# Kernel tuning notes

Measured on AMD Instinct MI355X. Metric: run time of the kernel, lower is better.

## Reference

```python
import jax, jax.numpy as jnp
import numpy as np

B, T, C = 2, 2048, 1024
NH = 16
HS = C // NH            # 64
BD = max(HS // 4, 16)   # 16
HORIZON = 32


def _windows(t, delta):
    # t: [B, nh, T, d] -> [B, nh, T, delta, d]; window w at pos i maps to original index i-delta+1+w
    padded = jnp.pad(t, ((0, 0), (0, 0), (delta - 1, 0), (0, 0)))
    idx = jnp.arange(t.shape[2])[:, None] + jnp.arange(delta)[None, :]
    return padded[:, :, idx]


def setup_inputs() -> dict:
    key = jax.random.key(0)
    ks = jax.random.split(key, 16)
    s = 0.02
    inp = {
        "x": jax.random.normal(ks[0], (B, T, C), dtype=jnp.float32),
        # weights stored [in, out] (transposed vs torch Linear)
        "w_disp": jax.random.normal(ks[1], (C, NH * BD), dtype=jnp.float32) * s,
        "b_disp": jnp.zeros((NH * BD,), dtype=jnp.float32),
        "w_val": jax.random.normal(ks[2], (C, C), dtype=jnp.float32) * s,
        "b_val": jnp.zeros((C,), dtype=jnp.float32),
        "rel_pos_emb": jax.random.normal(ks[3], (HORIZON, BD), dtype=jnp.float32) * s,
        "w_state": jax.random.normal(ks[4], (BD, BD), dtype=jnp.float32) * s,
        "b_state": jnp.zeros((BD,), dtype=jnp.float32),
        "w_strain": jax.random.normal(ks[5], (BD, BD), dtype=jnp.float32) * s,
        "b_strain": jnp.zeros((BD,), dtype=jnp.float32),
        "w_state_i": jax.random.normal(ks[6], (BD, BD), dtype=jnp.float32) * s,
        "w_state_j": jax.random.normal(ks[7], (BD, BD), dtype=jnp.float32) * s,
        "w_pos": jax.random.normal(ks[8], (BD, BD), dtype=jnp.float32) * s,
        "w_bond_out": jax.random.normal(ks[9], (BD, 1), dtype=jnp.float32) * s,
        "b_bond_out": jnp.zeros((1,), dtype=jnp.float32),
        "w_damage": jax.random.normal(ks[10], (BD, BD), dtype=jnp.float32) * s,
        "b_damage": jnp.zeros((BD,), dtype=jnp.float32),
        "w_damage_out": jax.random.normal(ks[11], (BD, 1), dtype=jnp.float32) * s,
        "b_damage_out": jnp.full((1,), -3.0, dtype=jnp.float32),
        "w_cproj": jax.random.normal(ks[12], (C, C), dtype=jnp.float32) * s,
        "b_cproj": jnp.zeros((C,), dtype=jnp.float32),
    }
    return inp


def reference(x, w_disp, b_disp, w_val, b_val, rel_pos_emb, w_state, b_state,
              w_strain, b_strain, w_state_i, w_state_j, w_pos,
              w_bond_out, b_bond_out, w_damage, b_damage,
              w_damage_out, b_damage_out, w_cproj, b_cproj):
    Bx, Tx, Cx = x.shape
    delta = min(HORIZON, Tx)
    gelu = lambda v: jax.nn.gelu(v, approximate=False)

    disp = (x @ w_disp + b_disp).reshape(Bx, Tx, NH, BD).transpose(0, 2, 1, 3)   # [B,nh,T,bd]
    val = (x @ w_val + b_val).reshape(Bx, Tx, NH, HS).transpose(0, 2, 1, 3)      # [B,nh,T,hs]

    disp_win = _windows(disp, delta)    # [B,nh,T,delta,bd]
    val_win = _windows(val, delta)      # [B,nh,T,delta,hs]

    cmask = (jnp.arange(Tx)[:, None] - delta + 1 + jnp.arange(delta)[None, :]) >= 0  # [T,delta]
    cmask_f = cmask.astype(x.dtype)

    strain = disp_win - disp[:, :, :, None, :]                                   # [B,nh,T,delta,bd]
    strain_for_state = strain @ w_state + b_state
    valid_counts = jnp.clip(cmask_f.sum(axis=-1), 1.0)                           # [T]
    state = (strain_for_state * cmask_f[None, None, :, :, None]).sum(axis=3) \
            / valid_counts[None, None, :, None]                                  # [B,nh,T,bd]
    state_win = _windows(state, delta)                                           # [B,nh,T,delta,bd]

    rel_emb = rel_pos_emb[:delta]                                                # [delta,bd]
    bond_act = gelu(strain @ w_strain + b_strain
                    + state[:, :, :, None, :] @ w_state_i
                    + state_win @ w_state_j
                    + rel_emb @ w_pos)                                           # [B,nh,T,delta,bd]
    bond_logits = (bond_act @ w_bond_out)[..., 0] + b_bond_out[0]                # [B,nh,T,delta]

    damage_act = gelu(strain @ w_damage + b_damage)
    damage = jax.nn.sigmoid((damage_act @ w_damage_out)[..., 0] + b_damage_out[0])

    logits = bond_logits - damage * 10.0
    logits = jnp.where(cmask[None, None], logits, -jnp.inf)
    weights = jax.nn.softmax(logits, axis=-1)                                    # [B,nh,T,delta]

    out = jnp.einsum('bntd,bntde->bnte', weights, val_win)                       # [B,nh,T,hs]
    out = out.transpose(0, 2, 1, 3).reshape(Bx, Tx, Cx)
    return out @ w_cproj + b_cproj
```

## Files before the change

### kernel.cpp

```cpp
#include <hip/hip_runtime.h>
#include <hip/hip_bf16.h>
#include <math.h>

constexpr int B_ = 2, T_ = 2048, C_ = 1024, NH_ = 16, HS_ = 64, BD_ = 16, DELTA_ = 32;
constexpr int M_ = B_ * T_;

typedef __bf16 bf16_t;
typedef __bf16 bf16x8 __attribute__((ext_vector_type(8)));
typedef float  f32x4  __attribute__((ext_vector_type(4)));

__device__ __forceinline__ float gelu_f(float x) {
    const float u = 0.7978845608028654f * (x + 0.044715f * x * x * x);
    const float e = __expf(2.0f * u);
    const float th = 1.0f - 2.0f / (e + 1.0f);
    return 0.5f * x * (1.0f + th);
}

__global__ __launch_bounds__(256) void convert_bf16_kernel(
    const float* __restrict__ in, bf16_t* __restrict__ out, int n)
{
    const int i = (blockIdx.x * 256 + threadIdx.x) * 8;
    if (i >= n) return;
    const float4 v0 = *(const float4*)(in + i);
    const float4 v1 = *(const float4*)(in + i + 4);
    bf16x8 o;
    o[0] = (bf16_t)v0.x; o[1] = (bf16_t)v0.y; o[2] = (bf16_t)v0.z; o[3] = (bf16_t)v0.w;
    o[4] = (bf16_t)v1.x; o[5] = (bf16_t)v1.y; o[6] = (bf16_t)v1.z; o[7] = (bf16_t)v1.w;
    *(bf16x8*)(out + i) = o;
}

__global__ __launch_bounds__(256) void transpose_w_kernel(
    const float* __restrict__ in, bf16_t* __restrict__ out, int K, int N)
{
    __shared__ float tile[32][33];
    const int n0 = blockIdx.x * 32, k0 = blockIdx.y * 32;
    const int tx = threadIdx.x & 31, ty = threadIdx.x >> 5;
    #pragma unroll
    for (int i = 0; i < 4; ++i)
        tile[ty + 8 * i][tx] = in[(size_t)(k0 + ty + 8 * i) * N + n0 + tx];
    __syncthreads();
    #pragma unroll
    for (int i = 0; i < 4; ++i)
        out[(size_t)(n0 + ty + 8 * i) * K + k0 + tx] = (bf16_t)tile[tx][ty + 8 * i];
}

__device__ __forceinline__ void gload16(const void* g, void* l) {
    __builtin_amdgcn_global_load_lds(
        (__attribute__((address_space(1))) void*)(g),
        (__attribute__((address_space(3))) void*)(l), 16, 0, 0);
}

#define GBM 128
#define GBN 64
#define GBK 32
__global__ __launch_bounds__(256) void gemm_bf16_async(
    const bf16_t* __restrict__ A, const bf16_t* __restrict__ Bt,
    const float* __restrict__ bias, float* __restrict__ C,
    int M, int N, int K)
{
    __shared__ __align__(16) bf16_t Al[GBM][GBK];
    __shared__ __align__(16) bf16_t Bl[GBN][GBK];
    const int tid  = threadIdx.x;
    const int lane = tid & 63;
    const int w    = tid >> 6;
    const int wr   = w >> 1, wc = w & 1;
    const int bm   = blockIdx.y * GBM, bn = blockIdx.x * GBN;

    const int lrow = lane >> 2;
    const int lcol = (lane & 3) * 8;
    const bf16_t* Ag0 = A  + (size_t)(bm + w * 32 + lrow) * K + lcol;
    const bf16_t* Ag1 = Ag0 + (size_t)16 * K;
    const bf16_t* Bg  = Bt + (size_t)(bn + w * 16 + lrow) * K + lcol;

    f32x4 acc[4][2] = {};

    for (int k0 = 0; k0 < K; k0 += GBK) {
        gload16(Ag0 + k0, &Al[w * 32][0]);
        gload16(Ag1 + k0, &Al[w * 32 + 16][0]);
        gload16(Bg  + k0, &Bl[w * 16][0]);
        __syncthreads();
        bf16x8 af[4], bf2[2];
        #pragma unroll
        for (int i = 0; i < 4; ++i)
            af[i] = *(const bf16x8*)&Al[wr * 64 + i * 16 + (lane & 15)][(lane >> 4) * 8];
        #pragma unroll
        for (int j = 0; j < 2; ++j)
            bf2[j] = *(const bf16x8*)&Bl[wc * 32 + j * 16 + (lane & 15)][(lane >> 4) * 8];
        #pragma unroll
        for (int i = 0; i < 4; ++i)
            #pragma unroll
            for (int j = 0; j < 2; ++j)
                acc[i][j] = __builtin_amdgcn_mfma_f32_16x16x32_bf16(af[i], bf2[j], acc[i][j], 0, 0, 0);
        __syncthreads();
    }

    #pragma unroll
    for (int i = 0; i < 4; ++i) {
        const int r0 = bm + wr * 64 + i * 16 + (lane >> 4) * 4;
        #pragma unroll
        for (int j = 0; j < 2; ++j) {
            const int c = bn + wc * 32 + j * 16 + (lane & 15);
            const float bv = bias[c];
            float* cp = C + (size_t)r0 * N + c;
            #pragma unroll
            for (int q = 0; q < 4; ++q)
                cp[(size_t)q * N] = acc[i][j][q] + bv;
        }
    }
}

#define PCT 128
__global__ __launch_bounds__(256) void precomp_kernel(
    const float* __restrict__ disp,
    const float* __restrict__ w_state, const float* __restrict__ b_state,
    const float* __restrict__ w_strain, const float* __restrict__ b_strain,
    const float* __restrict__ w_state_i, const float* __restrict__ w_state_j,
    const float* __restrict__ w_damage,
    float* __restrict__ P1, float* __restrict__ Q1, float* __restrict__ P2)
{
    __shared__ float s_d[PCT + 31][20];
    __shared__ float s_mv[PCT][20];
    __shared__ float s_st[PCT][20];
    __shared__ float s_wst[16][16], s_wstr[16][16], s_wsi[16][16], s_wsj[16][16], s_wdmg[16][16];
    __shared__ float s_bst[16], s_bstr[16];

    const int bid = blockIdx.x;
    const int tile = bid & (T_ / PCT - 1);
    const int h    = (bid >> 4) & 15;
    const int b    = bid >> 8;
    const int t0   = tile * PCT;
    const int tid  = threadIdx.x;

    s_wst[tid >> 4][tid & 15]  = w_state[tid];
    s_wstr[tid >> 4][tid & 15] = w_strain[tid];
    s_wsi[tid >> 4][tid & 15]  = w_state_i[tid];
    s_wsj[tid >> 4][tid & 15]  = w_state_j[tid];
    s_wdmg[tid >> 4][tid & 15] = w_damage[tid];
    if (tid < 16) { s_bst[tid] = b_state[tid]; s_bstr[tid] = b_strain[tid]; }

    for (int it = tid; it < (PCT + 31) * 4; it += 256) {
        const int row = it >> 2, q = it & 3;
        int rg = t0 - 31 + row; if (rg < 0) rg = 0;
        *(float4*)&s_d[row][q * 4] =
            *(const float4*)(disp + (size_t)(b * T_ + rg) * 256 + h * 16 + q * 4);
    }
    __syncthreads();

    #pragma unroll
    for (int p = 0; p < 8; ++p) {
        const int it = p * 256 + tid;
        const int tl = it >> 4, e = it & 15;
        const int t = t0 + tl;
        const int dlo = max(0, 31 - t);
        float s = 0.0f;
        for (int d = dlo; d < 32; ++d) s += s_d[tl + d][e];
        s_mv[tl][e] = s / (float)(32 - dlo) - s_d[tl + 31][e];
    }
    __syncthreads();

    #pragma unroll
    for (int p = 0; p < 8; ++p) {
        const int it = p * 256 + tid;
        const int tl = it >> 4, e = it & 15;
        float a = s_bst[e];
        #pragma unroll
        for (int k = 0; k < 16; ++k) a += s_mv[tl][k] * s_wst[k][e];
        s_st[tl][e] = a;
    }
    __syncthreads();

    #pragma unroll
    for (int p = 0; p < 8; ++p) {
        const int it = p * 256 + tid;
        const int tl = it >> 4, e = it & 15;
        float d1 = 0.0f, p2 = 0.0f, sj = 0.0f, si = 0.0f;
        #pragma unroll
        for (int k = 0; k < 16; ++k) {
            const float dv = s_d[tl + 31][k];
            const float sv = s_st[tl][k];
            d1 += dv * s_wstr[k][e];
            p2 += dv * s_wdmg[k][e];
            sj += sv * s_wsj[k][e];
            si += sv * s_wsi[k][e];
        }
        const size_t o = (size_t)(b * T_ + t0 + tl) * 256 + h * 16 + e;
        P1[o] = d1 + sj;
        Q1[o] = s_bstr[e] + si - d1;
        P2[o] = p2;
    }
}

__global__ __launch_bounds__(256) void attn_kernel(
    const float* __restrict__ P1, const float* __restrict__ Q1,
    const float* __restrict__ P2, const float* __restrict__ val,
    const float* __restrict__ rel_pos_emb, const float* __restrict__ w_pos,
    const float* __restrict__ w_bond_out, const float* __restrict__ b_bond_out,
    const float* __restrict__ b_damage,
    const float* __restrict__ w_damage_out, const float* __restrict__ b_damage_out,
    bf16_t* __restrict__ att)
{
    __shared__ float sP1[95][20], sP2[95][20], sQ1[64][20];
    __shared__ float sVal[95][68];
    __shared__ float sWv[64][33];
    __shared__ float s_relw[32][20];
    __shared__ float s_wb[16], s_wd[16], s_bd[16];

    const int tid  = threadIdx.x;
    const int bid  = blockIdx.x;
    const int tile = bid & 31;
    const int h    = (bid >> 5) & 15;
    const int b    = bid >> 9;
    const int t0   = tile * 64;

    for (int it = tid; it < 95 * 4; it += 256) {
        const int row = it >> 2, q = it & 3;
        int rg = t0 - 31 + row; if (rg < 0) rg = 0;
        const size_t o = (size_t)(b * T_ + rg) * 256 + h * 16 + q * 4;
        *(float4*)&sP1[row][q * 4] = *(const float4*)(P1 + o);
        *(float4*)&sP2[row][q * 4] = *(const float4*)(P2 + o);
    }
    {
        const int row = tid >> 2, q = tid & 3;
        *(float4*)&sQ1[row][q * 4] =
            *(const float4*)(Q1 + (size_t)(b * T_ + t0 + row) * 256 + h * 16 + q * 4);
    }
    for (int it = tid; it < 95 * 16; it += 256) {
        const int row = it >> 4, q = it & 15;
        int rg = t0 - 31 + row; if (rg < 0) rg = 0;
        *(float4*)&sVal[row][q * 4] =
            *(const float4*)(val + (size_t)(b * T_ + rg) * 1024 + h * 64 + q * 4);
    }
    {
        for (int it = tid; it < 512; it += 256) {
            const int dd = it >> 4, ee = it & 15;
            float a = 0.0f;
            #pragma unroll
            for (int k = 0; k < 16; ++k) a += rel_pos_emb[dd * 16 + k] * w_pos[k * 16 + ee];
            s_relw[dd][ee] = a;
        }
        if (tid < 16) {
            s_wb[tid] = w_bond_out[tid];
            s_wd[tid] = w_damage_out[tid];
            s_bd[tid] = b_damage[tid];
        }
    }
    __syncthreads();

    const int lane = tid & 63;
    const int w    = tid >> 6;
    const int half = lane >> 5;
    const int d    = lane & 31;
    const float bb  = b_bond_out[0];
    const float bdo = b_damage_out[0];

    #pragma unroll
    for (int pp = 0; pp < 8; ++pp) {
        const int p  = (w << 3) + pp;
        const int tl = (p << 1) + half;
        const int i  = tl + d;
        const bool valid = (t0 - 31 + i) >= 0;

        float bacc = 0.0f, dacc = 0.0f;
        #pragma unroll
        for (int q = 0; q < 4; ++q) {
            const float4 q1  = *(const float4*)&sQ1[tl][q * 4];
            const float4 p2t = *(const float4*)&sP2[tl + 31][q * 4];
            const float4 p1r = *(const float4*)&sP1[i][q * 4];
            const float4 p2r = *(const float4*)&sP2[i][q * 4];
            const float4 rw  = *(const float4*)&s_relw[d][q * 4];
            bacc += gelu_f(p1r.x + q1.x + rw.x) * s_wb[4 * q + 0];
            bacc += gelu_f(p1r.y + q1.y + rw.y) * s_wb[4 * q + 1];
            bacc += gelu_f(p1r.z + q1.z + rw.z) * s_wb[4 * q + 2];
            bacc += gelu_f(p1r.w + q1.w + rw.w) * s_wb[4 * q + 3];
            dacc += gelu_f(p2r.x - p2t.x + s_bd[4 * q + 0]) * s_wd[4 * q + 0];
            dacc += gelu_f(p2r.y - p2t.y + s_bd[4 * q + 1]) * s_wd[4 * q + 1];
            dacc += gelu_f(p2r.z - p2t.z + s_bd[4 * q + 2]) * s_wd[4 * q + 2];
            dacc += gelu_f(p2r.w - p2t.w + s_bd[4 * q + 3]) * s_wd[4 * q + 3];
        }

        float logit = -INFINITY;
        if (valid) {
            const float damage = 1.0f / (1.0f + __expf(-(dacc + bdo)));
            logit = bacc + bb - 10.0f * damage;
        }
        float m = logit;
        #pragma unroll
        for (int off = 16; off; off >>= 1) m = fmaxf(m, __shfl_xor(m, off, 32));
        const float pe = valid ? __expf(logit - m) : 0.0f;
        float ss = pe;
        #pragma unroll
        for (int off = 16; off; off >>= 1) ss += __shfl_xor(ss, off, 32);
        sWv[tl][d] = pe / ss;
    }

    #pragma unroll
    for (int pp = 0; pp < 8; ++pp) {
        const int tl0 = (w << 4) + (pp << 1);
        float acc0 = 0.0f, acc1 = 0.0f;
        #pragma unroll
        for (int j = 0; j < 33; ++j) {
            const float v = sVal[tl0 + j][lane];
            if (j < 32) acc0 += sWv[tl0][j] * v;
            if (j >= 1) acc1 += sWv[tl0 + 1][j - 1] * v;
        }
        const size_t o = (size_t)(b * T_ + t0 + tl0) * 1024 + h * 64 + lane;
        att[o]        = (bf16_t)acc0;
        att[o + 1024] = (bf16_t)acc1;
    }
}

extern "C" void kernel_launch(void* const* d_in, const int* in_sizes, int n_in,
                              void* d_out, int out_size, void* d_ws, size_t ws_size,
                              hipStream_t stream)
{
    const float* x        = (const float*)d_in[0];
    const float* w_disp   = (const float*)d_in[1];
    const float* b_disp   = (const float*)d_in[2];
    const float* w_val    = (const float*)d_in[3];
    const float* b_val    = (const float*)d_in[4];
    const float* rel      = (const float*)d_in[5];
    const float* w_state  = (const float*)d_in[6];
    const float* b_state  = (const float*)d_in[7];
    const float* w_strain = (const float*)d_in[8];
    const float* b_strain = (const float*)d_in[9];
    const float* w_si     = (const float*)d_in[10];
    const float* w_sj     = (const float*)d_in[11];
    const float* w_pos    = (const float*)d_in[12];
    const float* w_bond   = (const float*)d_in[13];
    const float* b_bond   = (const float*)d_in[14];
    const float* w_dmg    = (const float*)d_in[15];
    const float* b_dmg    = (const float*)d_in[16];
    const float* w_dout   = (const float*)d_in[17];
    const float* b_dout   = (const float*)d_in[18];
    const float* w_cproj  = (const float*)d_in[19];
    const float* b_cproj  = (const float*)d_in[20];

    float* out = (float*)d_out;
    float* ws  = (float*)d_ws;

    const size_t R = (size_t)M_ * 256;
    float* disp = ws;
    float* P1   = ws + R;
    float* Q1   = ws + 2 * R;
    float* P2   = ws + 3 * R;
    float* val  = ws + 4 * R;
    bf16_t* xb   = (bf16_t*)(ws + 8 * R);
    bf16_t* attb = xb;
    bf16_t* wdT  = (bf16_t*)(ws + 10 * R);
    bf16_t* wvT  = wdT + (size_t)256 * 1024;
    bf16_t* wcT  = wvT + (size_t)1024 * 1024;

    convert_bf16_kernel<<<(M_ * C_) / (256 * 8), 256, 0, stream>>>(x, xb, M_ * C_);
    transpose_w_kernel<<<dim3(256 / 32, C_ / 32), 256, 0, stream>>>(w_disp, wdT, C_, 256);
    transpose_w_kernel<<<dim3(C_ / 32, C_ / 32), 256, 0, stream>>>(w_val, wvT, C_, C_);
    transpose_w_kernel<<<dim3(C_ / 32, C_ / 32), 256, 0, stream>>>(w_cproj, wcT, C_, C_);

    gemm_bf16_async<<<dim3(256 / GBN, M_ / GBM), 256, 0, stream>>>(xb, wdT, b_disp, disp, M_, 256, C_);
    gemm_bf16_async<<<dim3(C_ / GBN, M_ / GBM), 256, 0, stream>>>(xb, wvT, b_val, val, M_, C_, C_);

    precomp_kernel<<<B_ * NH_ * (T_ / PCT), 256, 0, stream>>>(
        disp, w_state, b_state, w_strain, b_strain, w_si, w_sj, w_dmg, P1, Q1, P2);

    attn_kernel<<<B_ * NH_ * (T_ / 64), 256, 0, stream>>>(
        P1, Q1, P2, val, rel, w_pos, w_bond, b_bond, b_dmg, w_dout, b_dout, attb);

    gemm_bf16_async<<<dim3(C_ / GBN, M_ / GBM), 256, 0, stream>>>(attb, wcT, b_cproj, out, M_, C_, C_);
}
```

Measured before the change: 265.7 us.

## Double-buffer GEMMs, fuse disp/val GEMMs and transposes, use fast exp/rcp intrinsics

The GEMM now uses 128x128 tiles, double-buffered LDS with async prefetch of the next K tile, and an XCD-aware block remap. The disp and val projections become one launch, and the three weight transposes become one launch. GELU, sigmoid, softmax and the divisions switch to hardware exp2 and rcp intrinsics, with GELU rewritten in the form x*sigmoid. This cuts launch overhead, global-memory stalls and transcendental cost, at the price of doubling LDS use and slightly lower numerical precision.

```diff
diff --git a/kernel.cpp b/kernel.cpp
--- a/kernel.cpp
+++ b/kernel.cpp
@@ -9,12 +9,17 @@
 typedef __bf16 bf16x8 __attribute__((ext_vector_type(8)));
 typedef float  f32x4  __attribute__((ext_vector_type(4)));
 
+__device__ __forceinline__ float frcp(float x)  { return __builtin_amdgcn_rcpf(x); }
+__device__ __forceinline__ float fexp2(float x) { return __builtin_amdgcn_exp2f(x); }
+
 __device__ __forceinline__ float gelu_f(float x) {
-    const float u = 0.7978845608028654f * (x + 0.044715f * x * x * x);
-    const float e = __expf(2.0f * u);
-    const float th = 1.0f - 2.0f / (e + 1.0f);
-    return 0.5f * x * (1.0f + th);
-}
+    const float x2  = x * x;
+    const float arg = x * fmaf(0.10294321f, x2, 2.3022074f);
+    const float e   = fexp2(arg);
+    const float r   = frcp(e + 1.0f);
+    return x - x * r;
+}
+constexpr float LOG2E = 1.4426950409f;
 
 __global__ __launch_bounds__(256) void convert_bf16_kernel(
     const float* __restrict__ in, bf16_t* __restrict__ out, int n)
@@ -29,9 +34,17 @@
     *(bf16x8*)(out + i) = o;
 }
 
-__global__ __launch_bounds__(256) void transpose_w_kernel(
-    const float* __restrict__ in, bf16_t* __restrict__ out, int K, int N)
-{
+__global__ __launch_bounds__(256) void transpose3_kernel(
+    const float* __restrict__ w_val, const float* __restrict__ w_cproj,
+    const float* __restrict__ w_disp,
+    bf16_t* __restrict__ wvT, bf16_t* __restrict__ wcT, bf16_t* __restrict__ wdT)
+{
+    const int z = blockIdx.z;
+    const float* in; bf16_t* out; int K = 1024, N = 1024;
+    if (z == 0)      { in = w_val;   out = wvT; }
+    else if (z == 1) { in = w_cproj; out = wcT; }
+    else             { in = w_disp;  out = wdT; N = 256; if (blockIdx.x >= 8) return; }
+
     __shared__ float tile[32][33];
     const int n0 = blockIdx.x * 32, k0 = blockIdx.y * 32;
     const int tx = threadIdx.x & 31, ty = threadIdx.x >> 5;
@@ -51,55 +64,67 @@
 }
 
 #define GBM 128
-#define GBN 64
+#define GBN 128
 #define GBK 32
-__global__ __launch_bounds__(256) void gemm_bf16_async(
+
+__device__ __forceinline__ void gemm_core(
+    bf16_t (*Al)[GBM][GBK], bf16_t (*Bl)[GBN][GBK],
     const bf16_t* __restrict__ A, const bf16_t* __restrict__ Bt,
     const float* __restrict__ bias, float* __restrict__ C,
-    int M, int N, int K)
-{
-    __shared__ __align__(16) bf16_t Al[GBM][GBK];
-    __shared__ __align__(16) bf16_t Bl[GBN][GBK];
+    int N, int K, int bm, int bn)
+{
     const int tid  = threadIdx.x;
     const int lane = tid & 63;
     const int w    = tid >> 6;
     const int wr   = w >> 1, wc = w & 1;
-    const int bm   = blockIdx.y * GBM, bn = blockIdx.x * GBN;
 
     const int lrow = lane >> 2;
     const int lcol = (lane & 3) * 8;
     const bf16_t* Ag0 = A  + (size_t)(bm + w * 32 + lrow) * K + lcol;
     const bf16_t* Ag1 = Ag0 + (size_t)16 * K;
-    const bf16_t* Bg  = Bt + (size_t)(bn + w * 16 + lrow) * K + lcol;
-
-    f32x4 acc[4][2] = {};
-
-    for (int k0 = 0; k0 < K; k0 += GBK) {
-        gload16(Ag0 + k0, &Al[w * 32][0]);
-        gload16(Ag1 + k0, &Al[w * 32 + 16][0]);
-        gload16(Bg  + k0, &Bl[w * 16][0]);
-        __syncthreads();
-        bf16x8 af[4], bf2[2];
+    const bf16_t* Bg0 = Bt + (size_t)(bn + w * 32 + lrow) * K + lcol;
+    const bf16_t* Bg1 = Bg0 + (size_t)16 * K;
+
+    f32x4 acc[4][4] = {};
+    const int nt = K / GBK;
+    int cur = 0;
+
+    gload16(Ag0, &Al[0][w * 32][0]);
+    gload16(Ag1, &Al[0][w * 32 + 16][0]);
+    gload16(Bg0, &Bl[0][w * 32][0]);
+    gload16(Bg1, &Bl[0][w * 32 + 16][0]);
+    __syncthreads();
+
+    for (int t = 0; t < nt; ++t) {
+        if (t + 1 < nt) {
+            const int k1 = (t + 1) * GBK;
+            gload16(Ag0 + k1, &Al[cur ^ 1][w * 32][0]);
+            gload16(Ag1 + k1, &Al[cur ^ 1][w * 32 + 16][0]);
+            gload16(Bg0 + k1, &Bl[cur ^ 1][w * 32][0]);
+            gload16(Bg1 + k1, &Bl[cur ^ 1][w * 32 + 16][0]);
+        }
+        bf16x8 af[4], bfr[4];
         #pragma unroll
         for (int i = 0; i < 4; ++i)
-            af[i] = *(const bf16x8*)&Al[wr * 64 + i * 16 + (lane & 15)][(lane >> 4) * 8];
-        #pragma unroll
-        for (int j = 0; j < 2; ++j)
-            bf2[j] = *(const bf16x8*)&Bl[wc * 32 + j * 16 + (lane & 15)][(lane >> 4) * 8];
+            af[i] = *(const bf16x8*)&Al[cur][wr * 64 + i * 16 + (lane & 15)][(lane >> 4) * 8];
+        #pragma unroll
+        for (int j = 0; j < 4; ++j)
+            bfr[j] = *(const bf16x8*)&Bl[cur][wc * 64 + j * 16 + (lane & 15)][(lane >> 4) * 8];
         #pragma unroll
         for (int i = 0; i < 4; ++i)
             #pragma unroll
-            for (int j = 0; j < 2; ++j)
-                acc[i][j] = __builtin_amdgcn_mfma_f32_16x16x32_bf16(af[i], bf2[j], acc[i][j], 0, 0, 0);
+            for (int j = 0; j < 4; ++j)
+                acc[i][j] = __builtin_amdgcn_mfma_f32_16x16x32_bf16(af[i], bfr[j], acc[i][j], 0, 0, 0);
         __syncthreads();
+        cur ^= 1;
     }
 
     #pragma unroll
     for (int i = 0; i < 4; ++i) {
         const int r0 = bm + wr * 64 + i * 16 + (lane >> 4) * 4;
         #pragma unroll
-        for (int j = 0; j < 2; ++j) {
-            const int c = bn + wc * 32 + j * 16 + (lane & 15);
+        for (int j = 0; j < 4; ++j) {
+            const int c = bn + wc * 64 + j * 16 + (lane & 15);
             const float bv = bias[c];
             float* cp = C + (size_t)r0 * N + c;
             #pragma unroll
@@ -107,6 +132,40 @@
                 cp[(size_t)q * N] = acc[i][j][q] + bv;
         }
     }
+}
+
+__global__ __launch_bounds__(256) void gemm_bf16_db(
+    const bf16_t* __restrict__ A, const bf16_t* __restrict__ Bt,
+    const float* __restrict__ bias, float* __restrict__ C,
+    int M, int N, int K)
+{
+    __shared__ __align__(16) bf16_t Al[2][GBM][GBK];
+    __shared__ __align__(16) bf16_t Bl[2][GBN][GBK];
+    const int gx  = gridDim.x;
+    const int nwg = gx * gridDim.y;
+    const int bid = blockIdx.y * gx + blockIdx.x;
+    const int wid = (bid & 7) * (nwg >> 3) + (bid >> 3);
+    const int bx  = wid % gx, by = wid / gx;
+    gemm_core(Al, Bl, A, Bt, bias, C, N, K, by * GBM, bx * GBN);
+}
+
+__global__ __launch_bounds__(256) void gemm_dv_fused(
+    const bf16_t* __restrict__ A,
+    const bf16_t* __restrict__ wvT, const bf16_t* __restrict__ wdT,
+    const float* __restrict__ b_val, const float* __restrict__ b_disp,
+    float* __restrict__ val, float* __restrict__ disp)
+{
+    __shared__ __align__(16) bf16_t Al[2][GBM][GBK];
+    __shared__ __align__(16) bf16_t Bl[2][GBN][GBK];
+    const int gx  = 10;
+    const int nwg = 320;
+    const int bid = blockIdx.y * gx + blockIdx.x;
+    const int wid = (bid & 7) * (nwg >> 3) + (bid >> 3);
+    const int bx  = wid % gx, by = wid / gx;
+    if (bx < 8)
+        gemm_core(Al, Bl, A, wvT, b_val, val, 1024, 1024, by * GBM, bx * GBN);
+    else
+        gemm_core(Al, Bl, A, wdT, b_disp, disp, 256, 1024, by * GBM, (bx - 8) * GBN);
 }
 
 #define PCT 128
@@ -154,7 +213,7 @@
         const int dlo = max(0, 31 - t);
         float s = 0.0f;
         for (int d = dlo; d < 32; ++d) s += s_d[tl + d][e];
-        s_mv[tl][e] = s / (float)(32 - dlo) - s_d[tl + 31][e];
+        s_mv[tl][e] = s * frcp((float)(32 - dlo)) - s_d[tl + 31][e];
     }
     __syncthreads();
 
@@ -280,17 +339,17 @@
 
         float logit = -INFINITY;
         if (valid) {
-            const float damage = 1.0f / (1.0f + __expf(-(dacc + bdo)));
+            const float damage = frcp(1.0f + fexp2(-LOG2E * (dacc + bdo)));
             logit = bacc + bb - 10.0f * damage;
         }
         float m = logit;
         #pragma unroll
         for (int off = 16; off; off >>= 1) m = fmaxf(m, __shfl_xor(m, off, 32));
-        const float pe = valid ? __expf(logit - m) : 0.0f;
+        const float pe = valid ? fexp2(LOG2E * (logit - m)) : 0.0f;
         float ss = pe;
         #pragma unroll
         for (int off = 16; off; off >>= 1) ss += __shfl_xor(ss, off, 32);
-        sWv[tl][d] = pe / ss;
+        sWv[tl][d] = pe * frcp(ss);
     }
 
     #pragma unroll
@@ -351,12 +410,9 @@
     bf16_t* wcT  = wvT + (size_t)1024 * 1024;
 
     convert_bf16_kernel<<<(M_ * C_) / (256 * 8), 256, 0, stream>>>(x, xb, M_ * C_);
-    transpose_w_kernel<<<dim3(256 / 32, C_ / 32), 256, 0, stream>>>(w_disp, wdT, C_, 256);
-    transpose_w_kernel<<<dim3(C_ / 32, C_ / 32), 256, 0, stream>>>(w_val, wvT, C_, C_);
-    transpose_w_kernel<<<dim3(C_ / 32, C_ / 32), 256, 0, stream>>>(w_cproj, wcT, C_, C_);
-
-    gemm_bf16_async<<<dim3(256 / GBN, M_ / GBM), 256, 0, stream>>>(xb, wdT, b_disp, disp, M_, 256, C_);
-    gemm_bf16_async<<<dim3(C_ / GBN, M_ / GBM), 256, 0, stream>>>(xb, wvT, b_val, val, M_, C_, C_);
+    transpose3_kernel<<<dim3(32, 32, 3), 256, 0, stream>>>(w_val, w_cproj, w_disp, wvT, wcT, wdT);
+
+    gemm_dv_fused<<<dim3(10, 32), 256, 0, stream>>>(xb, wvT, wdT, b_val, b_disp, val, disp);
 
     precomp_kernel<<<B_ * NH_ * (T_ / PCT), 256, 0, stream>>>(
         disp, w_state, b_state, w_strain, b_strain, w_si, w_sj, w_dmg, P1, Q1, P2);
@@ -364,5 +420,5 @@
     attn_kernel<<<B_ * NH_ * (T_ / 64), 256, 0, stream>>>(
         P1, Q1, P2, val, rel, w_pos, w_bond, b_bond, b_dmg, w_dout, b_dout, attb);
 
-    gemm_bf16_async<<<dim3(C_ / GBN, M_ / GBM), 256, 0, stream>>>(attb, wcT, b_cproj, out, M_, C_, C_);
-}
+    gemm_bf16_db<<<dim3(C_ / GBN, M_ / GBM), 256, 0, stream>>>(attb, wcT, b_cproj, out, M_, C_, C_);
+}
```

Measured after the change: 224.3 us. -15.6%, faster.
